# Kernel optimization log

Hardware: AMD Instinct MI355X
Metric: run time of the kernel (lower is better)

The kernel has to match this reference:

```python
import jax, jax.numpy as jnp
import numpy as np

N_EXPERTS = 8
EMB = 1024
HID = 2816


def setup_inputs() -> dict:
    key = jax.random.key(0)
    k1, k2, k3, k4, k5 = jax.random.split(key, 5)
    x = jax.random.normal(k1, (2, 2048, EMB), dtype=jnp.float32)
    w_router = jax.random.normal(k2, (EMB, N_EXPERTS), dtype=jnp.float32) * 0.02
    w1 = jax.random.normal(k3, (N_EXPERTS, EMB, HID), dtype=jnp.float32) * 0.02
    w3 = jax.random.normal(k4, (N_EXPERTS, EMB, HID), dtype=jnp.float32) * 0.02
    w2 = jax.random.normal(k5, (N_EXPERTS, HID, EMB), dtype=jnp.float32) * 0.02
    return {"x": x, "w_router": w_router, "w1": w1, "w3": w3, "w2": w2,
            "n_experts_per_token": 2}


def reference(x, w_router, w1, w3, w2, n_experts_per_token):
    # x: (b, s, d) -> flatten to tokens (t, d)
    orig_shape = x.shape
    xf = x.reshape(-1, orig_shape[-1])                      # (t, d)
    scores = xf @ w_router                                  # (t, E)
    top_v, top_i = jax.lax.top_k(scores, n_experts_per_token)  # (t, k)
    top_p = jax.nn.softmax(top_v, axis=-1)                  # (t, k)
    # dense per-token gate over experts (top-k indices are distinct)
    gates = jnp.sum(jax.nn.one_hot(top_i, w_router.shape[-1], dtype=x.dtype)
                    * top_p[..., None], axis=1)             # (t, E)
    # SwiGLU for every expert (dense reference for the masked dispatch)
    h = jnp.einsum('td,edh->teh', xf, w1)                   # (t, E, H)
    g = jnp.einsum('td,edh->teh', xf, w3)                   # (t, E, H)
    expert_out = jnp.einsum('teh,ehd->ted', jax.nn.silu(h) * g, w2)  # (t, E, d)
    y = jnp.einsum('ted,te->td', expert_out, gates)
    return y.reshape(orig_shape)
```

## Files before the change

kernel.cpp:

```cpp
#include <hip/hip_runtime.h>
#include <hip/hip_bf16.h>

#define N_EXPERTS 8
#define EMB 1024
#define HID 2816
#define NTOK 4096
#define NSLOT (NTOK * 2)
#define TLIST NTOK

typedef float f32x4 __attribute__((ext_vector_type(4)));
typedef short short8 __attribute__((ext_vector_type(8)));

static __device__ __forceinline__ unsigned short f2bf(float v) {
    __hip_bfloat16 b = __float2bfloat16(v);
    return *reinterpret_cast<unsigned short*>(&b);
}

static __device__ __forceinline__ void ldst16(const unsigned short* g, unsigned short* l) {
    __builtin_amdgcn_global_load_lds(
        (const __attribute__((address_space(1))) unsigned int*)g,
        (__attribute__((address_space(3))) unsigned int*)l,
        16, 0, 0);
}

__global__ __launch_bounds__(256) void transpose_cvt(const float* __restrict__ in,
                                                     unsigned short* __restrict__ out,
                                                     int R, int C) {
    __shared__ unsigned short tile[64][68];
    int e = blockIdx.z;
    int r0 = blockIdx.y * 64, c0 = blockIdx.x * 64;
    const float* src = in + (size_t)e * R * C;
    unsigned short* dst = out + (size_t)e * R * C;
    int tid = threadIdx.x;
#pragma unroll
    for (int i = 0; i < 4; ++i) {
        int lin = i * 256 + tid;
        int r = lin >> 4, c4 = (lin & 15) * 4;
        float4 v = *(const float4*)&src[(size_t)(r0 + r) * C + c0 + c4];
        ushort4 b;
        b.x = f2bf(v.x); b.y = f2bf(v.y); b.z = f2bf(v.z); b.w = f2bf(v.w);
        *(ushort4*)&tile[r][c4] = b;
    }
    __syncthreads();
#pragma unroll
    for (int i = 0; i < 4; ++i) {
        int lin = i * 256 + tid;
        int c = lin >> 4, r4 = (lin & 15) * 4;
        ushort4 b;
        b.x = tile[r4 + 0][c]; b.y = tile[r4 + 1][c];
        b.z = tile[r4 + 2][c]; b.w = tile[r4 + 3][c];
        *(ushort4*)&dst[(size_t)(c0 + c) * R + r0 + r4] = b;
    }
}

__global__ __launch_bounds__(64) void router_kernel(const float* __restrict__ x,
                                                    const float* __restrict__ wr,
                                                    unsigned short* __restrict__ xbf,
                                                    int* __restrict__ sel,
                                                    float* __restrict__ gates) {
    int t = blockIdx.x, lane = threadIdx.x;
    const float* xr = x + (size_t)t * EMB;
    float acc[N_EXPERTS];
#pragma unroll
    for (int e = 0; e < N_EXPERTS; ++e) acc[e] = 0.f;
    for (int d = lane; d < EMB; d += 64) {
        float xv = xr[d];
        xbf[(size_t)t * EMB + d] = f2bf(xv);
        const float* w = wr + d * N_EXPERTS;
#pragma unroll
        for (int e = 0; e < N_EXPERTS; ++e) acc[e] += xv * w[e];
    }
#pragma unroll
    for (int off = 32; off; off >>= 1) {
#pragma unroll
        for (int e = 0; e < N_EXPERTS; ++e) acc[e] += __shfl_xor(acc[e], off, 64);
    }
    if (lane == 0) {
        int b0 = 0; float v0 = acc[0];
#pragma unroll
        for (int e = 1; e < N_EXPERTS; ++e) if (acc[e] > v0) { v0 = acc[e]; b0 = e; }
        int b1 = -1; float v1 = -1e30f;
#pragma unroll
        for (int e = 0; e < N_EXPERTS; ++e) if (e != b0 && acc[e] > v1) { v1 = acc[e]; b1 = e; }
        float g0 = 1.f / (1.f + expf(v1 - v0));
        float g1 = 1.f - g0;
        sel[t] = b0 | (b1 << 8);
        gates[2 * t] = g0;
        gates[2 * t + 1] = g1;
    }
}

__global__ __launch_bounds__(256) void build_lists(const int* __restrict__ sel,
                                                   int* __restrict__ counts,
                                                   int* __restrict__ lists) {
    int e = blockIdx.x;
    int tid = threadIdx.x, lane = tid & 63, wid = tid >> 6;
    __shared__ int wsum[4];
    __shared__ int running;
    if (tid == 0) running = 0;
    __syncthreads();
    for (int base = 0; base < NTOK; base += 256) {
        int tok = base + tid;
        int s = sel[tok];
        int e0 = s & 0xff, e1 = (s >> 8) & 0xff;
        bool take = (e0 == e) || (e1 == e);
        int slot = (e0 == e) ? 2 * tok : 2 * tok + 1;
        unsigned long long b = __ballot(take);
        int lp = __popcll(b & ((1ull << lane) - 1ull));
        if (lane == 0) wsum[wid] = __popcll(b);
        __syncthreads();
        int off = running;
        for (int w = 0; w < wid; ++w) off += wsum[w];
        if (take) lists[e * TLIST + off + lp] = slot;
        __syncthreads();
        if (tid == 0) running += wsum[0] + wsum[1] + wsum[2] + wsum[3];
        __syncthreads();
    }
    if (tid == 0) counts[e] = running;
}

__global__ __launch_bounds__(256) void gemm1_kernel(const unsigned short* __restrict__ xbf,
                                                    const unsigned short* __restrict__ w1T,
                                                    const unsigned short* __restrict__ w3T,
                                                    unsigned short* __restrict__ h,
                                                    const int* __restrict__ counts,
                                                    const int* __restrict__ lists) {
    int e = blockIdx.z;
    int cnt = counts[e];
    int rt = blockIdx.y;
    if (rt * 128 >= cnt) return;
    int n0 = blockIdx.x * 64;

    __shared__ unsigned short As[128 * 32];
    __shared__ unsigned short B1s[64 * 32];
    __shared__ unsigned short B3s[64 * 32];
    __shared__ int slotArr[128];

    int tid = threadIdx.x;
    if (tid < 128) {
        int r = rt * 128 + tid;
        slotArr[tid] = (r < cnt) ? lists[e * TLIST + r] : -1;
    }
    __syncthreads();

    int lane = tid & 63, wid = tid >> 6;
    int seg = lane >> 2, chunk = lane & 3;

    int rA0 = wid * 32 + seg, rA1 = wid * 32 + 16 + seg;
    int s0 = slotArr[rA0], s1 = slotArr[rA1];
    int t0 = s0 >= 0 ? (s0 >> 1) : 0, t1 = s1 >= 0 ? (s1 >> 1) : 0;
    const unsigned short* gA0 = xbf + (size_t)t0 * EMB + chunk * 8;
    const unsigned short* gA1 = xbf + (size_t)t1 * EMB + chunk * 8;
    int rB = n0 + wid * 16 + seg;
    const unsigned short* gB1 = w1T + ((size_t)e * HID + rB) * EMB + chunk * 8;
    const unsigned short* gB3 = w3T + ((size_t)e * HID + rB) * EMB + chunk * 8;
    unsigned short* lA0 = &As[wid * 1024];
    unsigned short* lA1 = &As[wid * 1024 + 512];
    unsigned short* lB1 = &B1s[wid * 512];
    unsigned short* lB3 = &B3s[wid * 512];

    int wr = wid >> 1, wc = wid & 1;
    int lrow = lane & 15, quad = lane >> 4;

    f32x4 zero4 = {0.f, 0.f, 0.f, 0.f};
    f32x4 acc1[4][2], acc3[4][2];
#pragma unroll
    for (int mt = 0; mt < 4; ++mt)
#pragma unroll
        for (int nt = 0; nt < 2; ++nt) { acc1[mt][nt] = zero4; acc3[mt][nt] = zero4; }

    const int KT = EMB / 32;
    for (int kt = 0; kt < KT; ++kt) {
        ldst16(gA0, lA0); ldst16(gA1, lA1);
        ldst16(gB1, lB1); ldst16(gB3, lB3);
        gA0 += 32; gA1 += 32; gB1 += 32; gB3 += 32;
        __builtin_amdgcn_s_waitcnt(0);
        __syncthreads();
        short8 af[4], b1f[2], b3f[2];
#pragma unroll
        for (int mt = 0; mt < 4; ++mt)
            af[mt] = *(const short8*)&As[(wr * 64 + mt * 16 + lrow) * 32 + quad * 8];
#pragma unroll
        for (int nt = 0; nt < 2; ++nt) {
            b1f[nt] = *(const short8*)&B1s[(wc * 32 + nt * 16 + lrow) * 32 + quad * 8];
            b3f[nt] = *(const short8*)&B3s[(wc * 32 + nt * 16 + lrow) * 32 + quad * 8];
        }
#pragma unroll
        for (int mt = 0; mt < 4; ++mt)
#pragma unroll
            for (int nt = 0; nt < 2; ++nt) {
                acc1[mt][nt] = __builtin_amdgcn_mfma_f32_16x16x32_bf16(af[mt], b1f[nt], acc1[mt][nt], 0, 0, 0);
                acc3[mt][nt] = __builtin_amdgcn_mfma_f32_16x16x32_bf16(af[mt], b3f[nt], acc3[mt][nt], 0, 0, 0);
            }
        __syncthreads();
    }

#pragma unroll
    for (int mt = 0; mt < 4; ++mt) {
#pragma unroll
        for (int i = 0; i < 4; ++i) {
            int r = wr * 64 + mt * 16 + quad * 4 + i;
            int slot = slotArr[r];
            if (slot < 0) continue;
#pragma unroll
            for (int nt = 0; nt < 2; ++nt) {
                float v1 = acc1[mt][nt][i];
                float v3 = acc3[mt][nt][i];
                float hv = v1 / (1.f + __expf(-v1)) * v3;
                int c = n0 + wc * 32 + nt * 16 + lrow;
                h[(size_t)slot * HID + c] = f2bf(hv);
            }
        }
    }
}

__global__ __launch_bounds__(256) void gemm2_kernel(const unsigned short* __restrict__ h,
                                                    const unsigned short* __restrict__ w2T,
                                                    float* __restrict__ oslot,
                                                    const int* __restrict__ counts,
                                                    const int* __restrict__ lists,
                                                    const float* __restrict__ gates) {
    int e = blockIdx.z;
    int cnt = counts[e];
    int rt = blockIdx.y;
    if (rt * 128 >= cnt) return;
    int n0 = blockIdx.x * 128;

    __shared__ unsigned short As[128 * 32];
    __shared__ unsigned short Bs[128 * 32];
    __shared__ int slotArr[128];

    int tid = threadIdx.x;
    if (tid < 128) {
        int r = rt * 128 + tid;
        slotArr[tid] = (r < cnt) ? lists[e * TLIST + r] : -1;
    }
    __syncthreads();

    int lane = tid & 63, wid = tid >> 6;
    int seg = lane >> 2, chunk = lane & 3;

    int rA0 = wid * 32 + seg, rA1 = wid * 32 + 16 + seg;
    int s0 = slotArr[rA0], s1 = slotArr[rA1];
    const unsigned short* gA0 = h + (size_t)(s0 < 0 ? 0 : s0) * HID + chunk * 8;
    const unsigned short* gA1 = h + (size_t)(s1 < 0 ? 0 : s1) * HID + chunk * 8;
    int rB0 = n0 + wid * 32 + seg, rB1 = rB0 + 16;
    const unsigned short* gB0 = w2T + ((size_t)e * EMB + rB0) * HID + chunk * 8;
    const unsigned short* gB1 = w2T + ((size_t)e * EMB + rB1) * HID + chunk * 8;
    unsigned short* lA0 = &As[wid * 1024];
    unsigned short* lA1 = &As[wid * 1024 + 512];
    unsigned short* lB0 = &Bs[wid * 1024];
    unsigned short* lB1 = &Bs[wid * 1024 + 512];

    int wr = wid >> 1, wc = wid & 1;
    int lrow = lane & 15, quad = lane >> 4;

    f32x4 zero4 = {0.f, 0.f, 0.f, 0.f};
    f32x4 acc[4][4];
#pragma unroll
    for (int mt = 0; mt < 4; ++mt)
#pragma unroll
        for (int nt = 0; nt < 4; ++nt) acc[mt][nt] = zero4;

    const int KT = HID / 32;
    for (int kt = 0; kt < KT; ++kt) {
        ldst16(gA0, lA0); ldst16(gA1, lA1);
        ldst16(gB0, lB0); ldst16(gB1, lB1);
        gA0 += 32; gA1 += 32; gB0 += 32; gB1 += 32;
        __builtin_amdgcn_s_waitcnt(0);
        __syncthreads();
        short8 af[4], bf[4];
#pragma unroll
        for (int mt = 0; mt < 4; ++mt)
            af[mt] = *(const short8*)&As[(wr * 64 + mt * 16 + lrow) * 32 + quad * 8];
#pragma unroll
        for (int nt = 0; nt < 4; ++nt)
            bf[nt] = *(const short8*)&Bs[(wc * 64 + nt * 16 + lrow) * 32 + quad * 8];
#pragma unroll
        for (int mt = 0; mt < 4; ++mt)
#pragma unroll
            for (int nt = 0; nt < 4; ++nt)
                acc[mt][nt] = __builtin_amdgcn_mfma_f32_16x16x32_bf16(af[mt], bf[nt], acc[mt][nt], 0, 0, 0);
        __syncthreads();
    }

#pragma unroll
    for (int mt = 0; mt < 4; ++mt) {
#pragma unroll
        for (int i = 0; i < 4; ++i) {
            int r = wr * 64 + mt * 16 + quad * 4 + i;
            int slot = slotArr[r];
            if (slot < 0) continue;
            float g = gates[slot];
#pragma unroll
            for (int nt = 0; nt < 4; ++nt) {
                int c = n0 + wc * 64 + nt * 16 + lrow;
                oslot[(size_t)slot * EMB + c] = g * acc[mt][nt][i];
            }
        }
    }
}

__global__ __launch_bounds__(256) void combine_kernel(const float* __restrict__ oslot,
                                                      float* __restrict__ out) {
    int gid = blockIdx.x * 256 + threadIdx.x;
    int t = gid / (EMB / 4);
    int r = gid % (EMB / 4);
    const float4* a = (const float4*)(oslot + (size_t)(2 * t) * EMB);
    const float4* b = (const float4*)(oslot + (size_t)(2 * t + 1) * EMB);
    float4 va = a[r], vb = b[r];
    float4 vo = {va.x + vb.x, va.y + vb.y, va.z + vb.z, va.w + vb.w};
    ((float4*)out)[gid] = vo;
}

extern "C" void kernel_launch(void* const* d_in, const int* in_sizes, int n_in,
                              void* d_out, int out_size, void* d_ws, size_t ws_size,
                              hipStream_t stream) {
    const float* x = (const float*)d_in[0];
    const float* wrout = (const float*)d_in[1];
    const float* w1 = (const float*)d_in[2];
    const float* w3 = (const float*)d_in[3];
    const float* w2 = (const float*)d_in[4];
    float* out = (float*)d_out;

    char* ws = (char*)d_ws;
    const size_t SW = (size_t)N_EXPERTS * EMB * HID * 2;
    const size_t SX = (size_t)NTOK * EMB * 2;
    const size_t SH = (size_t)NSLOT * HID * 2;
    const size_t SMETA = 256 + (size_t)N_EXPERTS * TLIST * 4 + (size_t)NSLOT * 4 + (size_t)NTOK * 4;
    const size_t NEEDED = 3 * SW + SX + SH + SMETA;
    if (ws_size < NEEDED) return;

    unsigned short* w1T = (unsigned short*)(ws);
    unsigned short* w3T = (unsigned short*)(ws + SW);
    unsigned short* w2T = (unsigned short*)(ws + 2 * SW);
    unsigned short* xbf = (unsigned short*)(ws + 3 * SW);
    unsigned short* hbuf = (unsigned short*)(ws + 3 * SW + SX);
    char* meta = ws + 3 * SW + SX + SH;
    int* counts = (int*)meta;
    int* lists = (int*)(meta + 256);
    float* gates = (float*)(meta + 256 + (size_t)N_EXPERTS * TLIST * 4);
    int* sel = (int*)(meta + 256 + (size_t)N_EXPERTS * TLIST * 4 + (size_t)NSLOT * 4);
    float* oslot = (float*)(ws);

    transpose_cvt<<<dim3(HID / 64, EMB / 64, N_EXPERTS), 256, 0, stream>>>(w1, w1T, EMB, HID);
    transpose_cvt<<<dim3(HID / 64, EMB / 64, N_EXPERTS), 256, 0, stream>>>(w3, w3T, EMB, HID);
    transpose_cvt<<<dim3(EMB / 64, HID / 64, N_EXPERTS), 256, 0, stream>>>(w2, w2T, HID, EMB);

    router_kernel<<<NTOK, 64, 0, stream>>>(x, wrout, xbf, sel, gates);
    build_lists<<<N_EXPERTS, 256, 0, stream>>>(sel, counts, lists);

    gemm1_kernel<<<dim3(HID / 64, NTOK / 128, N_EXPERTS), 256, 0, stream>>>(
        xbf, w1T, w3T, hbuf, counts, lists);
    gemm2_kernel<<<dim3(EMB / 128, NTOK / 128, N_EXPERTS), 256, 0, stream>>>(
        hbuf, w2T, oslot, counts, lists, gates);
    combine_kernel<<<NTOK * EMB / 4 / 256, 256, 0, stream>>>(oslot, out);
}
```

Baseline: 534.4 us.

## Widen gemm1 N tile, split-K gemm2 with bf16 partials, vectorize router and transpose

gemm1 now computes 128-column tiles (double the accumulators) with a two-blocks-per-CU launch bound, raising data reuse per A-tile load. gemm2 splits the hidden dimension into two halves, doubling its grid, and writes gated partial outputs as bf16 into two buffers. The combine kernel sums all four bf16 partials per token. The router uses float4 loads and the weight transpose transposes during the LDS write so the stores are wider. Trade-offs: extra rounding from bf16 partial outputs, higher register pressure in gemm1, and a workspace buffer whose size must cover both partial sets.

After: 566.5 us. 6.0% more time.

```diff
diff --git a/kernel.cpp b/kernel.cpp
--- a/kernel.cpp
+++ b/kernel.cpp
@@ -15,6 +15,10 @@
     __hip_bfloat16 b = __float2bfloat16(v);
     return *reinterpret_cast<unsigned short*>(&b);
 }
+static __device__ __forceinline__ float bf2f(unsigned short u) {
+    unsigned int w = ((unsigned int)u) << 16;
+    return __builtin_bit_cast(float, w);
+}
 
 static __device__ __forceinline__ void ldst16(const unsigned short* g, unsigned short* l) {
     __builtin_amdgcn_global_load_lds(
@@ -26,7 +30,7 @@
 __global__ __launch_bounds__(256) void transpose_cvt(const float* __restrict__ in,
                                                      unsigned short* __restrict__ out,
                                                      int R, int C) {
-    __shared__ unsigned short tile[64][68];
+    __shared__ unsigned short tileT[64][68];
     int e = blockIdx.z;
     int r0 = blockIdx.y * 64, c0 = blockIdx.x * 64;
     const float* src = in + (size_t)e * R * C;
@@ -37,19 +41,21 @@
         int lin = i * 256 + tid;
         int r = lin >> 4, c4 = (lin & 15) * 4;
         float4 v = *(const float4*)&src[(size_t)(r0 + r) * C + c0 + c4];
-        ushort4 b;
-        b.x = f2bf(v.x); b.y = f2bf(v.y); b.z = f2bf(v.z); b.w = f2bf(v.w);
-        *(ushort4*)&tile[r][c4] = b;
+        tileT[c4 + 0][r] = f2bf(v.x);
+        tileT[c4 + 1][r] = f2bf(v.y);
+        tileT[c4 + 2][r] = f2bf(v.z);
+        tileT[c4 + 3][r] = f2bf(v.w);
     }
     __syncthreads();
 #pragma unroll
-    for (int i = 0; i < 4; ++i) {
+    for (int i = 0; i < 2; ++i) {
         int lin = i * 256 + tid;
-        int c = lin >> 4, r4 = (lin & 15) * 4;
-        ushort4 b;
-        b.x = tile[r4 + 0][c]; b.y = tile[r4 + 1][c];
-        b.z = tile[r4 + 2][c]; b.w = tile[r4 + 3][c];
-        *(ushort4*)&dst[(size_t)(c0 + c) * R + r0 + r4] = b;
+        int c = lin >> 3, r8 = (lin & 7) * 8;
+        ushort4 lo = *(const ushort4*)&tileT[c][r8];
+        ushort4 hi = *(const ushort4*)&tileT[c][r8 + 4];
+        unsigned short* d = &dst[(size_t)(c0 + c) * R + r0 + r8];
+        *(ushort4*)d = lo;
+        *(ushort4*)(d + 4) = hi;
     }
 }
 
@@ -63,12 +69,17 @@
     float acc[N_EXPERTS];
 #pragma unroll
     for (int e = 0; e < N_EXPERTS; ++e) acc[e] = 0.f;
-    for (int d = lane; d < EMB; d += 64) {
-        float xv = xr[d];
-        xbf[(size_t)t * EMB + d] = f2bf(xv);
-        const float* w = wr + d * N_EXPERTS;
-#pragma unroll
-        for (int e = 0; e < N_EXPERTS; ++e) acc[e] += xv * w[e];
+#pragma unroll
+    for (int it = 0; it < EMB / 256; ++it) {
+        int d4 = it * 256 + lane * 4;
+        float4 xv = *(const float4*)&xr[d4];
+        ushort4 b;
+        b.x = f2bf(xv.x); b.y = f2bf(xv.y); b.z = f2bf(xv.z); b.w = f2bf(xv.w);
+        *(ushort4*)&xbf[(size_t)t * EMB + d4] = b;
+        const float* w0 = wr + (size_t)d4 * N_EXPERTS;
+#pragma unroll
+        for (int e = 0; e < N_EXPERTS; ++e)
+            acc[e] += xv.x * w0[e] + xv.y * w0[8 + e] + xv.z * w0[16 + e] + xv.w * w0[24 + e];
     }
 #pragma unroll
     for (int off = 32; off; off >>= 1) {
@@ -119,21 +130,21 @@
     if (tid == 0) counts[e] = running;
 }
 
-__global__ __launch_bounds__(256) void gemm1_kernel(const unsigned short* __restrict__ xbf,
-                                                    const unsigned short* __restrict__ w1T,
-                                                    const unsigned short* __restrict__ w3T,
-                                                    unsigned short* __restrict__ h,
-                                                    const int* __restrict__ counts,
-                                                    const int* __restrict__ lists) {
+__global__ __launch_bounds__(256, 2) void gemm1_kernel(const unsigned short* __restrict__ xbf,
+                                                       const unsigned short* __restrict__ w1T,
+                                                       const unsigned short* __restrict__ w3T,
+                                                       unsigned short* __restrict__ h,
+                                                       const int* __restrict__ counts,
+                                                       const int* __restrict__ lists) {
     int e = blockIdx.z;
     int cnt = counts[e];
     int rt = blockIdx.y;
     if (rt * 128 >= cnt) return;
-    int n0 = blockIdx.x * 64;
+    int n0 = blockIdx.x * 128;
 
     __shared__ unsigned short As[128 * 32];
-    __shared__ unsigned short B1s[64 * 32];
-    __shared__ unsigned short B3s[64 * 32];
+    __shared__ unsigned short B1s[128 * 32];
+    __shared__ unsigned short B3s[128 * 32];
     __shared__ int slotArr[128];
 
     int tid = threadIdx.x;
@@ -151,44 +162,49 @@
     int t0 = s0 >= 0 ? (s0 >> 1) : 0, t1 = s1 >= 0 ? (s1 >> 1) : 0;
     const unsigned short* gA0 = xbf + (size_t)t0 * EMB + chunk * 8;
     const unsigned short* gA1 = xbf + (size_t)t1 * EMB + chunk * 8;
-    int rB = n0 + wid * 16 + seg;
-    const unsigned short* gB1 = w1T + ((size_t)e * HID + rB) * EMB + chunk * 8;
-    const unsigned short* gB3 = w3T + ((size_t)e * HID + rB) * EMB + chunk * 8;
+    int rB0 = n0 + wid * 32 + seg, rB1 = rB0 + 16;
+    const unsigned short* gB10 = w1T + ((size_t)e * HID + rB0) * EMB + chunk * 8;
+    const unsigned short* gB11 = w1T + ((size_t)e * HID + rB1) * EMB + chunk * 8;
+    const unsigned short* gB30 = w3T + ((size_t)e * HID + rB0) * EMB + chunk * 8;
+    const unsigned short* gB31 = w3T + ((size_t)e * HID + rB1) * EMB + chunk * 8;
     unsigned short* lA0 = &As[wid * 1024];
     unsigned short* lA1 = &As[wid * 1024 + 512];
-    unsigned short* lB1 = &B1s[wid * 512];
-    unsigned short* lB3 = &B3s[wid * 512];
+    unsigned short* lB10 = &B1s[wid * 1024];
+    unsigned short* lB11 = &B1s[wid * 1024 + 512];
+    unsigned short* lB30 = &B3s[wid * 1024];
+    unsigned short* lB31 = &B3s[wid * 1024 + 512];
 
     int wr = wid >> 1, wc = wid & 1;
     int lrow = lane & 15, quad = lane >> 4;
 
     f32x4 zero4 = {0.f, 0.f, 0.f, 0.f};
-    f32x4 acc1[4][2], acc3[4][2];
+    f32x4 acc1[4][4], acc3[4][4];
 #pragma unroll
     for (int mt = 0; mt < 4; ++mt)
 #pragma unroll
-        for (int nt = 0; nt < 2; ++nt) { acc1[mt][nt] = zero4; acc3[mt][nt] = zero4; }
+        for (int nt = 0; nt < 4; ++nt) { acc1[mt][nt] = zero4; acc3[mt][nt] = zero4; }
 
     const int KT = EMB / 32;
     for (int kt = 0; kt < KT; ++kt) {
         ldst16(gA0, lA0); ldst16(gA1, lA1);
-        ldst16(gB1, lB1); ldst16(gB3, lB3);
-        gA0 += 32; gA1 += 32; gB1 += 32; gB3 += 32;
+        ldst16(gB10, lB10); ldst16(gB11, lB11);
+        ldst16(gB30, lB30); ldst16(gB31, lB31);
+        gA0 += 32; gA1 += 32; gB10 += 32; gB11 += 32; gB30 += 32; gB31 += 32;
         __builtin_amdgcn_s_waitcnt(0);
         __syncthreads();
-        short8 af[4], b1f[2], b3f[2];
+        short8 af[4], b1f[4], b3f[4];
 #pragma unroll
         for (int mt = 0; mt < 4; ++mt)
             af[mt] = *(const short8*)&As[(wr * 64 + mt * 16 + lrow) * 32 + quad * 8];
 #pragma unroll
-        for (int nt = 0; nt < 2; ++nt) {
-            b1f[nt] = *(const short8*)&B1s[(wc * 32 + nt * 16 + lrow) * 32 + quad * 8];
-            b3f[nt] = *(const short8*)&B3s[(wc * 32 + nt * 16 + lrow) * 32 + quad * 8];
+        for (int nt = 0; nt < 4; ++nt) {
+            b1f[nt] = *(const short8*)&B1s[(wc * 64 + nt * 16 + lrow) * 32 + quad * 8];
+            b3f[nt] = *(const short8*)&B3s[(wc * 64 + nt * 16 + lrow) * 32 + quad * 8];
         }
 #pragma unroll
         for (int mt = 0; mt < 4; ++mt)
 #pragma unroll
-            for (int nt = 0; nt < 2; ++nt) {
+            for (int nt = 0; nt < 4; ++nt) {
                 acc1[mt][nt] = __builtin_amdgcn_mfma_f32_16x16x32_bf16(af[mt], b1f[nt], acc1[mt][nt], 0, 0, 0);
                 acc3[mt][nt] = __builtin_amdgcn_mfma_f32_16x16x32_bf16(af[mt], b3f[nt], acc3[mt][nt], 0, 0, 0);
             }
@@ -203,11 +219,11 @@
             int slot = slotArr[r];
             if (slot < 0) continue;
 #pragma unroll
-            for (int nt = 0; nt < 2; ++nt) {
+            for (int nt = 0; nt < 4; ++nt) {
                 float v1 = acc1[mt][nt][i];
                 float v3 = acc3[mt][nt][i];
                 float hv = v1 / (1.f + __expf(-v1)) * v3;
-                int c = n0 + wc * 32 + nt * 16 + lrow;
+                int c = n0 + wc * 64 + nt * 16 + lrow;
                 h[(size_t)slot * HID + c] = f2bf(hv);
             }
         }
@@ -216,7 +232,7 @@
 
 __global__ __launch_bounds__(256) void gemm2_kernel(const unsigned short* __restrict__ h,
                                                     const unsigned short* __restrict__ w2T,
-                                                    float* __restrict__ oslot,
+                                                    unsigned short* __restrict__ oslot,
                                                     const int* __restrict__ counts,
                                                     const int* __restrict__ lists,
                                                     const float* __restrict__ gates) {
@@ -224,7 +240,10 @@
     int cnt = counts[e];
     int rt = blockIdx.y;
     if (rt * 128 >= cnt) return;
-    int n0 = blockIdx.x * 128;
+    int bx = blockIdx.x;
+    int ks = bx >> 3;
+    int n0 = (bx & 7) * 128;
+    int k0 = ks * (HID / 2);
 
     __shared__ unsigned short As[128 * 32];
     __shared__ unsigned short Bs[128 * 32];
@@ -242,11 +261,11 @@
 
     int rA0 = wid * 32 + seg, rA1 = wid * 32 + 16 + seg;
     int s0 = slotArr[rA0], s1 = slotArr[rA1];
-    const unsigned short* gA0 = h + (size_t)(s0 < 0 ? 0 : s0) * HID + chunk * 8;
-    const unsigned short* gA1 = h + (size_t)(s1 < 0 ? 0 : s1) * HID + chunk * 8;
+    const unsigned short* gA0 = h + (size_t)(s0 < 0 ? 0 : s0) * HID + k0 + chunk * 8;
+    const unsigned short* gA1 = h + (size_t)(s1 < 0 ? 0 : s1) * HID + k0 + chunk * 8;
     int rB0 = n0 + wid * 32 + seg, rB1 = rB0 + 16;
-    const unsigned short* gB0 = w2T + ((size_t)e * EMB + rB0) * HID + chunk * 8;
-    const unsigned short* gB1 = w2T + ((size_t)e * EMB + rB1) * HID + chunk * 8;
+    const unsigned short* gB0 = w2T + ((size_t)e * EMB + rB0) * HID + k0 + chunk * 8;
+    const unsigned short* gB1 = w2T + ((size_t)e * EMB + rB1) * HID + k0 + chunk * 8;
     unsigned short* lA0 = &As[wid * 1024];
     unsigned short* lA1 = &As[wid * 1024 + 512];
     unsigned short* lB0 = &Bs[wid * 1024];
@@ -262,7 +281,7 @@
 #pragma unroll
         for (int nt = 0; nt < 4; ++nt) acc[mt][nt] = zero4;
 
-    const int KT = HID / 32;
+    const int KT = (HID / 2) / 32;
     for (int kt = 0; kt < KT; ++kt) {
         ldst16(gA0, lA0); ldst16(gA1, lA1);
         ldst16(gB0, lB0); ldst16(gB1, lB1);
@@ -284,6 +303,7 @@
         __syncthreads();
     }
 
+    unsigned short* ok = oslot + (size_t)ks * NSLOT * EMB;
 #pragma unroll
     for (int mt = 0; mt < 4; ++mt) {
 #pragma unroll
@@ -295,22 +315,39 @@
 #pragma unroll
             for (int nt = 0; nt < 4; ++nt) {
                 int c = n0 + wc * 64 + nt * 16 + lrow;
-                oslot[(size_t)slot * EMB + c] = g * acc[mt][nt][i];
+                ok[(size_t)slot * EMB + c] = f2bf(g * acc[mt][nt][i]);
             }
         }
     }
 }
 
-__global__ __launch_bounds__(256) void combine_kernel(const float* __restrict__ oslot,
+__global__ __launch_bounds__(256) void combine_kernel(const unsigned short* __restrict__ oslot,
                                                       float* __restrict__ out) {
     int gid = blockIdx.x * 256 + threadIdx.x;
-    int t = gid / (EMB / 4);
-    int r = gid % (EMB / 4);
-    const float4* a = (const float4*)(oslot + (size_t)(2 * t) * EMB);
-    const float4* b = (const float4*)(oslot + (size_t)(2 * t + 1) * EMB);
-    float4 va = a[r], vb = b[r];
-    float4 vo = {va.x + vb.x, va.y + vb.y, va.z + vb.z, va.w + vb.w};
-    ((float4*)out)[gid] = vo;
+    int t = gid / (EMB / 8);
+    int r8 = (gid % (EMB / 8)) * 8;
+    const unsigned short* p00 = oslot + (size_t)(2 * t) * EMB + r8;
+    const unsigned short* p01 = oslot + (size_t)(2 * t + 1) * EMB + r8;
+    const unsigned short* p10 = p00 + (size_t)NSLOT * EMB;
+    const unsigned short* p11 = p01 + (size_t)NSLOT * EMB;
+    short8 a = *(const short8*)p00, b = *(const short8*)p01;
+    short8 c = *(const short8*)p10, d = *(const short8*)p11;
+    float* o = out + (size_t)t * EMB + r8;
+    float4 lo, hi;
+#pragma unroll
+    for (int j = 0; j < 4; ++j) {
+        float v = bf2f((unsigned short)a[j]) + bf2f((unsigned short)b[j]) +
+                  bf2f((unsigned short)c[j]) + bf2f((unsigned short)d[j]);
+        ((float*)&lo)[j] = v;
+    }
+#pragma unroll
+    for (int j = 4; j < 8; ++j) {
+        float v = bf2f((unsigned short)a[j]) + bf2f((unsigned short)b[j]) +
+                  bf2f((unsigned short)c[j]) + bf2f((unsigned short)d[j]);
+        ((float*)&hi)[j - 4] = v;
+    }
+    *(float4*)o = lo;
+    *(float4*)(o + 4) = hi;
 }
 
 extern "C" void kernel_launch(void* const* d_in, const int* in_sizes, int n_in,
@@ -341,7 +378,7 @@
     int* lists = (int*)(meta + 256);
     float* gates = (float*)(meta + 256 + (size_t)N_EXPERTS * TLIST * 4);
     int* sel = (int*)(meta + 256 + (size_t)N_EXPERTS * TLIST * 4 + (size_t)NSLOT * 4);
-    float* oslot = (float*)(ws);
+    unsigned short* oslot = (unsigned short*)(ws);
 
     transpose_cvt<<<dim3(HID / 64, EMB / 64, N_EXPERTS), 256, 0, stream>>>(w1, w1T, EMB, HID);
     transpose_cvt<<<dim3(HID / 64, EMB / 64, N_EXPERTS), 256, 0, stream>>>(w3, w3T, EMB, HID);
@@ -350,9 +387,9 @@
     router_kernel<<<NTOK, 64, 0, stream>>>(x, wrout, xbf, sel, gates);
     build_lists<<<N_EXPERTS, 256, 0, stream>>>(sel, counts, lists);
 
-    gemm1_kernel<<<dim3(HID / 64, NTOK / 128, N_EXPERTS), 256, 0, stream>>>(
+    gemm1_kernel<<<dim3(HID / 128, NTOK / 128, N_EXPERTS), 256, 0, stream>>>(
         xbf, w1T, w3T, hbuf, counts, lists);
-    gemm2_kernel<<<dim3(EMB / 128, NTOK / 128, N_EXPERTS), 256, 0, stream>>>(
+    gemm2_kernel<<<dim3(16, NTOK / 128, N_EXPERTS), 256, 0, stream>>>(
         hbuf, w2T, oslot, counts, lists, gates);
-    combine_kernel<<<NTOK * EMB / 4 / 256, 256, 0, stream>>>(oslot, out);
-}
+    combine_kernel<<<NTOK * EMB / 8 / 256, 256, 0, stream>>>(oslot, out);
+}
```
